# Kernel optimization log

Hardware: AMD Instinct MI355X
Metric: run time of the kernel (lower is better)

Reference implementation:

```python
import jax, jax.numpy as jnp
import numpy as np


def _lstm_dir(xz, Uh, reverse):
    """Run one LSTM direction. xz: [B,T,4U] = x@W + b precomputed. Uh: [U,4U].
    activation='sigmoid' (replaces tanh on candidate and cell output),
    recurrent_activation='sigmoid' (Keras default). Gate order: i, f, g, o."""
    B = xz.shape[0]
    units = Uh.shape[0]
    h0 = jnp.zeros((B, units), xz.dtype)
    c0 = jnp.zeros((B, units), xz.dtype)

    def step(carry, z_t):
        h, c = carry
        z = z_t + h @ Uh                      # [B,4U]
        i, f, g, o = jnp.split(z, 4, axis=-1)
        i = jax.nn.sigmoid(i)
        f = jax.nn.sigmoid(f)
        g = jax.nn.sigmoid(g)                 # activation='sigmoid'
        o = jax.nn.sigmoid(o)
        c = f * c + i * g
        h = o * jax.nn.sigmoid(c)             # output activation also sigmoid
        return (h, c), h

    xz_t = jnp.swapaxes(xz, 0, 1)             # [T,B,4U]
    _, hs = jax.lax.scan(step, (h0, c0), xz_t, reverse=reverse)
    return jnp.swapaxes(hs, 0, 1)             # [B,T,U], time-ordered


def setup_inputs() -> dict:
    key = jax.random.key(0)
    k1, k2, k3 = jax.random.split(key, 3)
    B, T, D = 16, 1024, 1024
    L, U = 5, 512
    x = jax.random.normal(k1, (B, T, D), dtype=jnp.float32)
    # Glorot-ish scaling to keep sigmoids out of deep saturation
    W = jax.random.normal(k2, (L, 2, D, 4 * U), dtype=jnp.float32) * 0.03
    Uh = jax.random.normal(k3, (L, 2, U, 4 * U), dtype=jnp.float32) * 0.03
    b = jnp.zeros((L, 2, 4 * U), dtype=jnp.float32)
    return {"x": x, "W": W, "Uh": Uh, "b": b}


def reference(x, W, Uh, b):
    y = x
    n_layers = W.shape[0]
    for l in range(n_layers):
        outs = []
        for d, rev in ((0, False), (1, True)):
            # input projection for all timesteps at once (one big GEMM)
            xz = jnp.einsum('bti,io->bto', y, W[l, d]) + b[l, d]
            outs.append(_lstm_dir(xz, Uh[l, d], rev))
        y = jnp.concatenate(outs, axis=-1)    # Bidirectional merge_mode='concat'
    return y
```

## Files before the change

kernel.cpp:

```cpp
#include <hip/hip_runtime.h>
#include <hip/hip_bf16.h>
#include <stdint.h>


typedef __attribute__((ext_vector_type(8))) short short8;
typedef __attribute__((ext_vector_type(4))) float f32x4;

union U128 { uint4 u; short8 s; };
static __device__ __forceinline__ short8 as_short8(uint4 v) { U128 x; x.u = v; return x.s; }

static __device__ __forceinline__ float sigf(float x) { return 1.0f / (1.0f + __expf(-x)); }

static __device__ __forceinline__ uint32_t f2bfbits(float f) {
  union { float f; uint32_t u; } x; x.f = f;
  return (x.u + 0x7fffu + ((x.u >> 16) & 1u)) >> 16;
}
static __device__ __forceinline__ float bflo(uint32_t v) {
  union { uint32_t u; float f; } x; x.u = v << 16; return x.f;
}
static __device__ __forceinline__ float bfhi(uint32_t v) {
  union { uint32_t u; float f; } x; x.u = v & 0xffff0000u; return x.f;
}
static __device__ __forceinline__ bool qok(unsigned long long v) {
  return ((uint32_t)v != 0u) & ((uint32_t)(v >> 32) != 0u);
}

__global__ __launch_bounds__(256) void f32_to_bf16_k(const float* __restrict__ in,
                                                     __hip_bfloat16* __restrict__ out,
                                                     int n4) {
  int i = blockIdx.x * 256 + threadIdx.x;
  if (i < n4) {
    float4 v = ((const float4*)in)[i];
    uint32_t lo = f2bfbits(v.x) | (f2bfbits(v.y) << 16);
    uint32_t hi = f2bfbits(v.z) | (f2bfbits(v.w) << 16);
    ((uint2*)out)[i] = make_uint2(lo, hi);
  }
}

__global__ __launch_bounds__(256) void transpose_bf16_k(const float* __restrict__ in,
                                                        __hip_bfloat16* __restrict__ outp,
                                                        int R) {
  __shared__ float tile[64][65];
  int d = blockIdx.z;
  int k0 = blockIdx.x * 64;
  int c0 = blockIdx.y * 64;
  const float* inb = in + (size_t)d * R * 2048;
  __hip_bfloat16* ob = outp + (size_t)d * 2048 * R;
  int col = threadIdx.x & 63, rr = threadIdx.x >> 6;
#pragma unroll
  for (int i = 0; i < 16; ++i) {
    int r = rr + i * 4;
    tile[r][col] = inb[(size_t)(k0 + r) * 2048 + c0 + col];
  }
  __syncthreads();
#pragma unroll
  for (int i = 0; i < 16; ++i) {
    int r = rr + i * 4;
    ob[(size_t)(c0 + r) * R + k0 + col] = __float2bfloat16(tile[col][r]);
  }
}

__global__ __launch_bounds__(256) void gemm_xz_k(const __hip_bfloat16* __restrict__ y,
                                                 const __hip_bfloat16* __restrict__ Wt,
                                                 const float* __restrict__ bias,
                                                 __hip_bfloat16* __restrict__ xz) {
  __shared__ uint4 Asl[8 * 2 * 64];
  __shared__ uint4 Bsl[8 * 2 * 64];
  int m0 = blockIdx.x * 128;
  int dir = blockIdx.y >> 4;
  int n0 = (blockIdx.y & 15) * 128;
  int tid = threadIdx.x, lane = tid & 63, wv = tid >> 6;
  int wm = wv & 1, wn = wv >> 1;
  const __hip_bfloat16* Wd = Wt + (size_t)dir * 2048 * 1024;
  f32x4 acc[4][4] = {};
  for (int kb = 0; kb < 1024; kb += 64) {
    __syncthreads();
#pragma unroll
    for (int i = 0; i < 4; ++i) {
      int slot = i * 256 + tid;
      int ln = slot & 63, kc = (slot >> 6) & 1, mt = slot >> 7;
      int row = mt * 16 + (ln & 15);
      int kk = kc * 32 + (ln >> 4) * 8;
      Asl[slot] = *(const uint4*)(y + (size_t)(m0 + row) * 1024 + kb + kk);
      Bsl[slot] = *(const uint4*)(Wd + (size_t)(n0 + row) * 1024 + kb + kk);
    }
    __syncthreads();
#pragma unroll
    for (int kc = 0; kc < 2; ++kc) {
      short8 af[4], bf[4];
#pragma unroll
      for (int i = 0; i < 4; ++i) {
        af[i] = as_short8(Asl[((wm * 4 + i) * 2 + kc) * 64 + lane]);
        bf[i] = as_short8(Bsl[((wn * 4 + i) * 2 + kc) * 64 + lane]);
      }
#pragma unroll
      for (int i = 0; i < 4; ++i)
#pragma unroll
        for (int j = 0; j < 4; ++j)
          acc[i][j] = __builtin_amdgcn_mfma_f32_16x16x32_bf16(af[i], bf[j], acc[i][j], 0, 0, 0);
    }
  }
  int cq = lane >> 4, cn = lane & 15;
#pragma unroll
  for (int i = 0; i < 4; ++i)
#pragma unroll
    for (int j = 0; j < 4; ++j) {
      int n_g = n0 + (wn * 4 + j) * 16 + cn;
      int q = n_g >> 9, u = n_g & 511, swg = u >> 5, jj = u & 31;
      float bv = bias[dir * 2048 + n_g];
#pragma unroll
      for (int r = 0; r < 4; ++r) {
        int m = m0 + (wm * 4 + i) * 16 + cq * 4 + r;
        int bb = m >> 10, t = m & 1023;
        size_t addr = (((size_t)(dir * 16 + swg) * 1024 + t) * 2048) + (q * 16 + bb) * 32 + jj;
        xz[addr] = __float2bfloat16(acc[i][j][r] + bv);
      }
    }
}

__global__ __launch_bounds__(256) void lstm_rec_k(const __hip_bfloat16* __restrict__ Ut,
                                                  const __hip_bfloat16* __restrict__ xz,
                                                  __hip_bfloat16* __restrict__ ynext,
                                                  float* __restrict__ outf,
                                                  const __hip_bfloat16* __restrict__ Wtn,
                                                  const float* __restrict__ biasn,
                                                  __hip_bfloat16* __restrict__ xznext) {
  extern __shared__ char smem[];
  int tid = threadIdx.x, lane = tid & 63, wv = tid >> 6;

  if (blockIdx.x < 32) {
    uint4* uh = (uint4*)smem;
    __hip_bfloat16* hbuf = (__hip_bfloat16*)(smem + 131072);
    float* zbuf = (float*)(smem + 147712);
    __hip_bfloat16* xbuf = (__hip_bfloat16*)(smem + 155904);
    int dir = blockIdx.x & 1;
    int swg = blockIdx.x >> 1;
    int u0 = swg * 32;
    int quad = lane >> 4, l15 = lane & 15;
    const __hip_bfloat16* Ud = Ut + (size_t)dir * 2048 * 512;

#pragma unroll 4
    for (int i = 0; i < 32; ++i) {
      int slot = i * 256 + tid;
      int ls = slot & 63, kc = (slot >> 6) & 15, nt = slot >> 10;
      int n_g = (nt >> 1) * 512 + u0 + (nt & 1) * 16 + (ls & 15);
      int k = kc * 32 + (ls >> 4) * 8;
      uh[slot] = *(const uint4*)(Ud + (size_t)n_g * 512 + k);
    }
    __syncthreads();

    int nt0 = wv * 2, nt1 = wv * 2 + 1;
    int pb = tid >> 4, pj = (tid & 15) * 2;
    float c0 = 0.f, c1 = 0.f;

    int t0 = dir ? 1023 : 0;
    const uint4* xp0 = (const uint4*)(xz + ((size_t)(dir * 16 + swg) * 1024 + t0) * 2048) + tid;
    uint4 xcur = *xp0;

    for (int s = 0; s < 1024; ++s) {
      int t = dir ? (1023 - s) : s;
      uint4 xnxt;
      if (s < 1023) {
        int tn = dir ? (1022 - s) : (s + 1);
        xnxt = *((const uint4*)(xz + ((size_t)(dir * 16 + swg) * 1024 + tn) * 2048) + tid);
      }
      f32x4 z0 = {}, z1 = {};
      if (s > 0) {
        int tprev = dir ? (t + 1) : (t - 1);
        unsigned long long hv[8];
        const unsigned long long* gp[8];
#pragma unroll
        for (int i = 0; i < 4; ++i) {
          int v = i * 2048 + tid * 8;
          int bb = v >> 9, col = v & 511;
          const unsigned long long* g =
              (const unsigned long long*)(ynext + ((size_t)bb * 1024 + tprev) * 1024 + dir * 512 + col);
          gp[2 * i] = g;
          gp[2 * i + 1] = g + 1;
        }
#pragma unroll
        for (int i = 0; i < 8; ++i)
          hv[i] = __hip_atomic_load(gp[i], __ATOMIC_RELAXED, __HIP_MEMORY_SCOPE_AGENT);
        for (;;) {
          bool ok = true;
#pragma unroll
          for (int i = 0; i < 8; ++i)
            ok &= ((uint32_t)hv[i] != 0u) && ((uint32_t)(hv[i] >> 32) != 0u);
          if (ok) break;
#pragma unroll
          for (int i = 0; i < 8; ++i)
            if (((uint32_t)hv[i] == 0u) || ((uint32_t)(hv[i] >> 32) == 0u))
              hv[i] = __hip_atomic_load(gp[i], __ATOMIC_RELAXED, __HIP_MEMORY_SCOPE_AGENT);
        }
#pragma unroll
        for (int i = 0; i < 4; ++i) {
          int v = i * 2048 + tid * 8;
          int bb = v >> 9, col = v & 511;
          unsigned long long* lp = (unsigned long long*)(hbuf + bb * 520 + col);
          lp[0] = hv[2 * i];
          lp[1] = hv[2 * i + 1];
        }
        __syncthreads();
#pragma unroll
        for (int kc = 0; kc < 16; ++kc) {
          short8 afrag = *(const short8*)(hbuf + l15 * 520 + kc * 32 + quad * 8);
          z0 = __builtin_amdgcn_mfma_f32_16x16x32_bf16(afrag, as_short8(uh[(nt0 * 16 + kc) * 64 + lane]), z0, 0, 0, 0);
          z1 = __builtin_amdgcn_mfma_f32_16x16x32_bf16(afrag, as_short8(uh[(nt1 * 16 + kc) * 64 + lane]), z1, 0, 0, 0);
        }
      }
#pragma unroll
      for (int r = 0; r < 4; ++r) {
        int m = quad * 4 + r;
        zbuf[m * 128 + nt0 * 16 + l15] = z0[r];
        zbuf[m * 128 + nt1 * 16 + l15] = z1[r];
      }
      *(uint4*)(xbuf + tid * 8) = xcur;
      __syncthreads();
      const float* zb = zbuf + pb * 128;
      uint32_t xi = *(const uint32_t*)(xbuf + (0 * 16 + pb) * 32 + pj);
      uint32_t xf = *(const uint32_t*)(xbuf + (1 * 16 + pb) * 32 + pj);
      uint32_t xg = *(const uint32_t*)(xbuf + (2 * 16 + pb) * 32 + pj);
      uint32_t xo = *(const uint32_t*)(xbuf + (3 * 16 + pb) * 32 + pj);
      float i0 = sigf(zb[pj] + bflo(xi)),      i1 = sigf(zb[pj + 1] + bfhi(xi));
      float f0 = sigf(zb[32 + pj] + bflo(xf)), f1 = sigf(zb[32 + pj + 1] + bfhi(xf));
      float g0 = sigf(zb[64 + pj] + bflo(xg)), g1 = sigf(zb[64 + pj + 1] + bfhi(xg));
      float o0 = sigf(zb[96 + pj] + bflo(xo)), o1 = sigf(zb[96 + pj + 1] + bfhi(xo));
      c0 = f0 * c0 + i0 * g0;
      c1 = f1 * c1 + i1 * g1;
      float h0 = o0 * sigf(c0);
      float h1 = o1 * sigf(c1);
      size_t oidx = ((size_t)pb * 1024 + t) * 1024 + dir * 512 + u0 + pj;
      uint32_t ha = f2bfbits(h0); ha += (ha == 0u);
      uint32_t hb = f2bfbits(h1); hb += (hb == 0u);
      uint32_t hp = ha | (hb << 16);
      __hip_atomic_store((uint32_t*)(ynext + oidx), hp, __ATOMIC_RELAXED, __HIP_MEMORY_SCOPE_AGENT);
      if (outf) { outf[oidx] = h0; outf[oidx + 1] = h1; }
      __syncthreads();
      xcur = xnxt;
    }
    return;
  }

  if (!xznext) return;
  uint4* Asl = (uint4*)smem;
  uint4* Bsl = ((uint4*)smem) + 1024;
  int gb = blockIdx.x - 32;
  int wm = wv & 1, wn = wv >> 1;
  for (int g = gb; g < 4096; g += 96) {
    int kq = g >> 6, inner = g & 63;
    int c = (kq & 1) ? (31 - (kq >> 1)) : (32 + (kq >> 1));
    int tt0 = c * 16;
    int bg = inner & 1, ngi = (inner >> 1) & 15, gdir = inner >> 5;
    int n0 = ngi * 128;
    const __hip_bfloat16* Wd = Wtn + (size_t)gdir * 2048 * 1024;
    {
      int rr = (tt0 + 15 > 1023 - tt0) ? (tt0 + 15) : (1023 - tt0);
      int tp = rr + 32; if (tp > 1023) tp = 1023;
      const uint32_t* pp = (const uint32_t*)(ynext + ((size_t)(bg * 8) * 1024 + tp) * 1024);
      while (__hip_atomic_load(pp, __ATOMIC_RELAXED, __HIP_MEMORY_SCOPE_AGENT) == 0u)
        __builtin_amdgcn_s_sleep(32);
    }
    f32x4 acc[4][4] = {};
    for (int kb = 0; kb < 1024; kb += 64) {
      __syncthreads();
#pragma unroll
      for (int i = 0; i < 4; ++i) {
        int slot = i * 256 + tid;
        int ln = slot & 63, kc = (slot >> 6) & 1, mt = slot >> 7;
        int row = mt * 16 + (ln & 15);
        int kcol = kc * 32 + (ln >> 4) * 8;
        int bb = bg * 8 + (row >> 4), tt = tt0 + (row & 15);
        const unsigned long long* ap =
            (const unsigned long long*)(ynext + ((size_t)bb * 1024 + tt) * 1024 + kb + kcol);
        unsigned long long a0 = __hip_atomic_load(ap, __ATOMIC_RELAXED, __HIP_MEMORY_SCOPE_AGENT);
        unsigned long long a1 = __hip_atomic_load(ap + 1, __ATOMIC_RELAXED, __HIP_MEMORY_SCOPE_AGENT);
        while (!(qok(a0) & qok(a1))) {
          __builtin_amdgcn_s_sleep(8);
          if (!qok(a0)) a0 = __hip_atomic_load(ap, __ATOMIC_RELAXED, __HIP_MEMORY_SCOPE_AGENT);
          if (!qok(a1)) a1 = __hip_atomic_load(ap + 1, __ATOMIC_RELAXED, __HIP_MEMORY_SCOPE_AGENT);
        }
        unsigned long long* asl = (unsigned long long*)&Asl[slot];
        asl[0] = a0; asl[1] = a1;
        Bsl[slot] = *(const uint4*)(Wd + (size_t)(n0 + row) * 1024 + kb + kcol);
      }
      __syncthreads();
#pragma unroll
      for (int kc = 0; kc < 2; ++kc) {
        short8 af[4], bf[4];
#pragma unroll
        for (int i = 0; i < 4; ++i) {
          af[i] = as_short8(Asl[((wm * 4 + i) * 2 + kc) * 64 + lane]);
          bf[i] = as_short8(Bsl[((wn * 4 + i) * 2 + kc) * 64 + lane]);
        }
#pragma unroll
        for (int i = 0; i < 4; ++i)
#pragma unroll
          for (int j = 0; j < 4; ++j)
            acc[i][j] = __builtin_amdgcn_mfma_f32_16x16x32_bf16(af[i], bf[j], acc[i][j], 0, 0, 0);
      }
    }
    int cq = lane >> 4, cn = lane & 15;
#pragma unroll
    for (int i = 0; i < 4; ++i)
#pragma unroll
      for (int j = 0; j < 4; ++j) {
        int n_g = n0 + (wn * 4 + j) * 16 + cn;
        int q = n_g >> 9, uu = n_g & 511, sw = uu >> 5, jj = uu & 31;
        float bv = biasn[gdir * 2048 + n_g];
#pragma unroll
        for (int r = 0; r < 4; ++r) {
          int ml = (wm * 4 + i) * 16 + cq * 4 + r;
          int bb = bg * 8 + (ml >> 4), tt = tt0 + (ml & 15);
          size_t addr = (((size_t)(gdir * 16 + sw) * 1024 + tt) * 2048) + (q * 16 + bb) * 32 + jj;
          xznext[addr] = __float2bfloat16(acc[i][j][r] + bv);
        }
      }
  }
}

extern "C" void kernel_launch(void* const* d_in, const int* in_sizes, int n_in,
                              void* d_out, int out_size, void* d_ws, size_t ws_size,
                              hipStream_t stream) {
  const float* x  = (const float*)d_in[0];
  const float* W  = (const float*)d_in[1];
  const float* Uh = (const float*)d_in[2];
  const float* b  = (const float*)d_in[3];

  char* ws = (char*)d_ws;
  size_t off = 0;
  __hip_bfloat16* yA  = (__hip_bfloat16*)(ws + off); off += (size_t)16 * 1024 * 1024 * 2;
  __hip_bfloat16* yB  = (__hip_bfloat16*)(ws + off); off += (size_t)16 * 1024 * 1024 * 2;
  __hip_bfloat16* xzA = (__hip_bfloat16*)(ws + off); off += (size_t)2 * 16 * 1024 * 2048 * 2;
  __hip_bfloat16* WtA = (__hip_bfloat16*)(ws + off); off += (size_t)2 * 2048 * 1024 * 2;
  __hip_bfloat16* UtA = (__hip_bfloat16*)(ws + off); off += (size_t)2 * 2048 * 512 * 2;
  __hip_bfloat16* xzB = (__hip_bfloat16*)(ws + off); off += (size_t)2 * 16 * 1024 * 2048 * 2;
  __hip_bfloat16* WtB = (__hip_bfloat16*)(ws + off); off += (size_t)2 * 2048 * 1024 * 2;
  __hip_bfloat16* UtB = (__hip_bfloat16*)(ws + off); off += (size_t)2 * 2048 * 512 * 2;
  const bool fuse = (ws_size >= off);

  f32_to_bf16_k<<<dim3(16384), dim3(256), 0, stream>>>(x, yA, 4194304);
  hipFuncSetAttribute(reinterpret_cast<const void*>(lstm_rec_k),
                      hipFuncAttributeMaxDynamicSharedMemorySize, 160000);

  if (!fuse) {
    for (int l = 0; l < 5; ++l) {
      transpose_bf16_k<<<dim3(16, 32, 2), dim3(256), 0, stream>>>(W + (size_t)l * 2 * 1024 * 2048, WtA, 1024);
      transpose_bf16_k<<<dim3(8, 32, 2),  dim3(256), 0, stream>>>(Uh + (size_t)l * 2 * 512 * 2048, UtA, 512);
      __hip_bfloat16* ycur = (l & 1) ? yB : yA;
      __hip_bfloat16* ynxt = (l & 1) ? yA : yB;
      hipMemsetAsync(ynxt, 0, (size_t)16 * 1024 * 1024 * 2, stream);
      gemm_xz_k<<<dim3(128, 32), dim3(256), 0, stream>>>(ycur, WtA, b + (size_t)l * 2 * 2048, xzA);
      lstm_rec_k<<<dim3(32), dim3(256), 160000, stream>>>(
          UtA, xzA, ynxt, (l == 4) ? (float*)d_out : nullptr, nullptr, nullptr, nullptr);
    }
    return;
  }

  __hip_bfloat16* Wtb[2] = {WtA, WtB};
  __hip_bfloat16* Utb[2] = {UtA, UtB};
  __hip_bfloat16* xzb[2] = {xzA, xzB};

  transpose_bf16_k<<<dim3(16, 32, 2), dim3(256), 0, stream>>>(W, Wtb[0], 1024);
  transpose_bf16_k<<<dim3(8, 32, 2),  dim3(256), 0, stream>>>(Uh, Utb[0], 512);
  hipMemsetAsync(yB, 0, (size_t)16 * 1024 * 1024 * 2, stream);
  gemm_xz_k<<<dim3(128, 32), dim3(256), 0, stream>>>(yA, Wtb[0], b, xzb[0]);

  for (int l = 0; l < 5; ++l) {
    __hip_bfloat16* ycur = (l & 1) ? yB : yA;
    __hip_bfloat16* ynxt = (l & 1) ? yA : yB;
    __hip_bfloat16* xzc  = xzb[l & 1];
    __hip_bfloat16* xzn  = xzb[(l + 1) & 1];
    if (l < 4)
      transpose_bf16_k<<<dim3(16, 32, 2), dim3(256), 0, stream>>>(
          W + (size_t)(l + 1) * 2 * 1024 * 2048, Wtb[(l + 1) & 1], 1024);
    int grid = (l < 4) ? 128 : 32;
    lstm_rec_k<<<dim3(grid), dim3(256), 160000, stream>>>(
        Utb[l & 1], xzc, ynxt, (l == 4) ? (float*)d_out : nullptr,
        (l < 4) ? Wtb[(l + 1) & 1] : nullptr,
        (l < 4) ? (b + (size_t)(l + 1) * 2 * 2048) : nullptr,
        (l < 4) ? xzn : nullptr);
    if (l < 4) {
      transpose_bf16_k<<<dim3(8, 32, 2), dim3(256), 0, stream>>>(
          Uh + (size_t)(l + 1) * 2 * 512 * 2048, Utb[(l + 1) & 1], 512);
      hipMemsetAsync(ycur, 0, (size_t)16 * 1024 * 1024 * 2, stream);
    }
  }
}
```

Before: 13.87 ms.

## Share single xz buffer in place with per-direction readiness waits

Drops the double-buffered xz/Wt/Ut workspaces and the non-fused fallback path, so the fused recurrent kernel writes the next layer's xz into the same buffer it is reading. The GEMM-side blocks now wait separately for the forward direction to pass t+47 and the backward direction to pass the mirrored step, which makes it safe to overwrite xz slices the recurrence has already consumed. Restrict qualifiers are removed from the aliased pointers. This cuts workspace use and makes the fused path run regardless of workspace size, at the cost of a tighter ordering dependency between the recurrence and the in-kernel projection.

```diff
diff --git a/kernel.cpp b/kernel.cpp
--- a/kernel.cpp
+++ b/kernel.cpp
@@ -119,12 +119,12 @@
 }
 
 __global__ __launch_bounds__(256) void lstm_rec_k(const __hip_bfloat16* __restrict__ Ut,
-                                                  const __hip_bfloat16* __restrict__ xz,
+                                                  const __hip_bfloat16* xz,
                                                   __hip_bfloat16* __restrict__ ynext,
                                                   float* __restrict__ outf,
                                                   const __hip_bfloat16* __restrict__ Wtn,
                                                   const float* __restrict__ biasn,
-                                                  __hip_bfloat16* __restrict__ xznext) {
+                                                  __hip_bfloat16* xznext) {
   extern __shared__ char smem[];
   int tid = threadIdx.x, lane = tid & 63, wv = tid >> 6;
 
@@ -254,10 +254,13 @@
     int n0 = ngi * 128;
     const __hip_bfloat16* Wd = Wtn + (size_t)gdir * 2048 * 1024;
     {
-      int rr = (tt0 + 15 > 1023 - tt0) ? (tt0 + 15) : (1023 - tt0);
-      int tp = rr + 32; if (tp > 1023) tp = 1023;
-      const uint32_t* pp = (const uint32_t*)(ynext + ((size_t)(bg * 8) * 1024 + tp) * 1024);
-      while (__hip_atomic_load(pp, __ATOMIC_RELAXED, __HIP_MEMORY_SCOPE_AGENT) == 0u)
+      int s0 = tt0 + 47;          if (s0 > 1023) s0 = 1023;
+      int s1 = (1023 - tt0) + 32; if (s1 > 1023) s1 = 1023;
+      const uint32_t* pp0 = (const uint32_t*)(ynext + ((size_t)(bg * 8) * 1024 + s0) * 1024);
+      const uint32_t* pp1 = (const uint32_t*)(ynext + ((size_t)(bg * 8) * 1024 + (1023 - s1)) * 1024 + 512);
+      while (__hip_atomic_load(pp0, __ATOMIC_RELAXED, __HIP_MEMORY_SCOPE_AGENT) == 0u)
+        __builtin_amdgcn_s_sleep(32);
+      while (__hip_atomic_load(pp1, __ATOMIC_RELAXED, __HIP_MEMORY_SCOPE_AGENT) == 0u)
         __builtin_amdgcn_s_sleep(32);
     }
     f32x4 acc[4][4] = {};
@@ -328,60 +331,36 @@
 
   char* ws = (char*)d_ws;
   size_t off = 0;
-  __hip_bfloat16* yA  = (__hip_bfloat16*)(ws + off); off += (size_t)16 * 1024 * 1024 * 2;
-  __hip_bfloat16* yB  = (__hip_bfloat16*)(ws + off); off += (size_t)16 * 1024 * 1024 * 2;
-  __hip_bfloat16* xzA = (__hip_bfloat16*)(ws + off); off += (size_t)2 * 16 * 1024 * 2048 * 2;
-  __hip_bfloat16* WtA = (__hip_bfloat16*)(ws + off); off += (size_t)2 * 2048 * 1024 * 2;
-  __hip_bfloat16* UtA = (__hip_bfloat16*)(ws + off); off += (size_t)2 * 2048 * 512 * 2;
-  __hip_bfloat16* xzB = (__hip_bfloat16*)(ws + off); off += (size_t)2 * 16 * 1024 * 2048 * 2;
-  __hip_bfloat16* WtB = (__hip_bfloat16*)(ws + off); off += (size_t)2 * 2048 * 1024 * 2;
-  __hip_bfloat16* UtB = (__hip_bfloat16*)(ws + off); off += (size_t)2 * 2048 * 512 * 2;
-  const bool fuse = (ws_size >= off);
+  __hip_bfloat16* yA = (__hip_bfloat16*)(ws + off); off += (size_t)16 * 1024 * 1024 * 2;
+  __hip_bfloat16* yB = (__hip_bfloat16*)(ws + off); off += (size_t)16 * 1024 * 1024 * 2;
+  __hip_bfloat16* xz = (__hip_bfloat16*)(ws + off); off += (size_t)2 * 16 * 1024 * 2048 * 2;
+  __hip_bfloat16* Wt = (__hip_bfloat16*)(ws + off); off += (size_t)2 * 2048 * 1024 * 2;
+  __hip_bfloat16* Ut = (__hip_bfloat16*)(ws + off); off += (size_t)2 * 2048 * 512 * 2;
 
   f32_to_bf16_k<<<dim3(16384), dim3(256), 0, stream>>>(x, yA, 4194304);
   hipFuncSetAttribute(reinterpret_cast<const void*>(lstm_rec_k),
                       hipFuncAttributeMaxDynamicSharedMemorySize, 160000);
 
-  if (!fuse) {
-    for (int l = 0; l < 5; ++l) {
-      transpose_bf16_k<<<dim3(16, 32, 2), dim3(256), 0, stream>>>(W + (size_t)l * 2 * 1024 * 2048, WtA, 1024);
-      transpose_bf16_k<<<dim3(8, 32, 2),  dim3(256), 0, stream>>>(Uh + (size_t)l * 2 * 512 * 2048, UtA, 512);
-      __hip_bfloat16* ycur = (l & 1) ? yB : yA;
-      __hip_bfloat16* ynxt = (l & 1) ? yA : yB;
-      hipMemsetAsync(ynxt, 0, (size_t)16 * 1024 * 1024 * 2, stream);
-      gemm_xz_k<<<dim3(128, 32), dim3(256), 0, stream>>>(ycur, WtA, b + (size_t)l * 2 * 2048, xzA);
-      lstm_rec_k<<<dim3(32), dim3(256), 160000, stream>>>(
-          UtA, xzA, ynxt, (l == 4) ? (float*)d_out : nullptr, nullptr, nullptr, nullptr);
-    }
-    return;
-  }
-
-  __hip_bfloat16* Wtb[2] = {WtA, WtB};
-  __hip_bfloat16* Utb[2] = {UtA, UtB};
-  __hip_bfloat16* xzb[2] = {xzA, xzB};
-
-  transpose_bf16_k<<<dim3(16, 32, 2), dim3(256), 0, stream>>>(W, Wtb[0], 1024);
-  transpose_bf16_k<<<dim3(8, 32, 2),  dim3(256), 0, stream>>>(Uh, Utb[0], 512);
+  transpose_bf16_k<<<dim3(16, 32, 2), dim3(256), 0, stream>>>(W, Wt, 1024);
+  transpose_bf16_k<<<dim3(8, 32, 2),  dim3(256), 0, stream>>>(Uh, Ut, 512);
   hipMemsetAsync(yB, 0, (size_t)16 * 1024 * 1024 * 2, stream);
-  gemm_xz_k<<<dim3(128, 32), dim3(256), 0, stream>>>(yA, Wtb[0], b, xzb[0]);
+  gemm_xz_k<<<dim3(128, 32), dim3(256), 0, stream>>>(yA, Wt, b, xz);
 
   for (int l = 0; l < 5; ++l) {
     __hip_bfloat16* ycur = (l & 1) ? yB : yA;
     __hip_bfloat16* ynxt = (l & 1) ? yA : yB;
-    __hip_bfloat16* xzc  = xzb[l & 1];
-    __hip_bfloat16* xzn  = xzb[(l + 1) & 1];
     if (l < 4)
       transpose_bf16_k<<<dim3(16, 32, 2), dim3(256), 0, stream>>>(
-          W + (size_t)(l + 1) * 2 * 1024 * 2048, Wtb[(l + 1) & 1], 1024);
+          W + (size_t)(l + 1) * 2 * 1024 * 2048, Wt, 1024);
     int grid = (l < 4) ? 128 : 32;
     lstm_rec_k<<<dim3(grid), dim3(256), 160000, stream>>>(
-        Utb[l & 1], xzc, ynxt, (l == 4) ? (float*)d_out : nullptr,
-        (l < 4) ? Wtb[(l + 1) & 1] : nullptr,
+        Ut, xz, ynxt, (l == 4) ? (float*)d_out : nullptr,
+        (l < 4) ? Wt : nullptr,
         (l < 4) ? (b + (size_t)(l + 1) * 2 * 2048) : nullptr,
-        (l < 4) ? xzn : nullptr);
+        (l < 4) ? xz : nullptr);
     if (l < 4) {
       transpose_bf16_k<<<dim3(8, 32, 2), dim3(256), 0, stream>>>(
-          Uh + (size_t)(l + 1) * 2 * 512 * 2048, Utb[(l + 1) & 1], 512);
+          Uh + (size_t)(l + 1) * 2 * 512 * 2048, Ut, 512);
       hipMemsetAsync(ycur, 0, (size_t)16 * 1024 * 1024 * 2, stream);
     }
   }
```

After: 16.12 ms. +16.2%, slower.
